# Kernel optimization log

Measured on AMD Instinct MI355X. Metric: run time of the kernel, lower is better.

The kernel has to match this reference:

```python
import jax, jax.numpy as jnp
import numpy as np

EPS = 1e-4      # geomloss: eps = blur**p = 0.01**2
N_ITERS = 20    # fixed Sinkhorn iterations
UNI_T = 2.0     # uniformity temperature (Wang & Isola)


def _sqdist(x, y):
    # [N,D],[M,D] -> [N,M] squared euclidean distances
    return jnp.sum((x[:, None, :] - y[None, :, :]) ** 2, axis=-1)


def _cost(x, y):
    # geomloss p=2 cost: ||x-y||^2 / 2
    return 0.5 * _sqdist(x, y)


def _softmin(C, h):
    # f_i = -eps * log( (1/M) * sum_j exp((h_j - C_ij)/eps) )
    M = C.shape[1]
    lse = jax.nn.logsumexp((h[None, :] - C) / EPS, axis=1)
    return -EPS * (lse - jnp.log(jnp.float32(M)))


def _sinkhorn_potentials(C):
    # alternating log-domain Sinkhorn updates, uniform weights
    def body(carry, _):
        f, g = carry
        f = _softmin(C, g)
        g = _softmin(C.T, f)
        return (f, g), None
    init = (jnp.zeros(C.shape[0], C.dtype), jnp.zeros(C.shape[1], C.dtype))
    (f, g), _ = jax.lax.scan(body, init, None, length=N_ITERS)
    return f, g


def _sym_potential(C):
    # symmetric fixed-point for the debiasing terms OT_eps(a,a)
    def body(p, _):
        return 0.5 * (p + _softmin(C, p)), None
    p, _ = jax.lax.scan(body, jnp.zeros(C.shape[0], C.dtype), None, length=N_ITERS)
    return p


def sinkhorn_divergence(x, y):
    # debiased: S = OT(x,y) - 0.5*OT(x,x) - 0.5*OT(y,y); envelope-theorem grads
    Cxy = _cost(x, y)
    f_d, g_d = _sinkhorn_potentials(jax.lax.stop_gradient(Cxy))
    f = _softmin(Cxy, jax.lax.stop_gradient(g_d))          # final differentiable step
    g = _softmin(Cxy.T, jax.lax.stop_gradient(f_d))

    Cxx = _cost(x, x)
    px = _sym_potential(jax.lax.stop_gradient(Cxx))
    fx = _softmin(Cxx, jax.lax.stop_gradient(px))          # 0.5*OT(x,x) = mean(fx)

    Cyy = _cost(y, y)
    py = _sym_potential(jax.lax.stop_gradient(Cyy))
    fy = _softmin(Cyy, jax.lax.stop_gradient(py))

    return jnp.mean(f) + jnp.mean(g) - jnp.mean(fx) - jnp.mean(fy)


def uniformity(x):
    # log E_{i != j} [ exp(-t * ||x_i - x_j||^2) ]
    N = x.shape[0]
    D = _sqdist(x, x)
    D = D + jnp.diag(jnp.full((N,), jnp.inf, dtype=x.dtype))  # mask self-pairs
    return jax.nn.logsumexp(-UNI_T * D) - jnp.log(jnp.float32(N * (N - 1)))


def setup_inputs() -> dict:
    key = jax.random.key(0)
    k1, k2 = jax.random.split(key)
    p_q = jax.random.normal(k1, (4096, 3), dtype=jnp.float32)
    p_gt = jax.random.normal(k2, (4096, 4), dtype=jnp.float32)
    return {"p_q": p_q, "p_gt": p_gt}


def reference(p_q, p_gt):
    L = sinkhorn_divergence(p_q, p_gt[:, :3])
    L = L + uniformity(p_q)
    return L
```

## Files before the change

### kernel.cpp

```cpp
#include <hip/hip_runtime.h>

#define NPT  4096
#define NBLK 256
#define NTHR 1024

constexpr float EPSV   = 1e-4f;
constexpr float LN2F   = 0.69314718055994531f;
constexpr float E2     = EPSV * LN2F;
constexpr float INV_E2 = 1.0f / E2;
constexpr float S_U    = 4.0f / LN2F;

#define SMEM_FLOATS 34816
#define SMEM_BYTES  (SMEM_FLOATS * 4)

#define WF     0
#define WG     4096
#define WPX0   8192
#define WPX1   12288
#define WPY0   16384
#define WPY1   20480
#define WFFIN  24576
#define WFXV   28672
#define WFYV   32768
#define WULS   36864
#define WCTR   40960
#define WREL   41472
#define WCNX   41984
#define WCNY   46080
#define WFG    50176
#define WGG    54272
#define WPXG0  58368
#define WPXG1  62464
#define WPYG0  66560
#define WPYG1  70656

typedef float v2f __attribute__((ext_vector_type(2)));

__device__ __forceinline__ float fexp2(float x) { return __builtin_amdgcn_exp2f(x); }
__device__ __forceinline__ float flog2(float x) { return __builtin_amdgcn_logf(x); }

__device__ __forceinline__ v2f pk_fma(v2f a, v2f b, v2f c) {
    v2f d;
    asm("v_pk_fma_f32 %0, %1, %2, %3" : "=v"(d) : "v"(a), "v"(b), "v"(c));
    return d;
}
__device__ __forceinline__ v2f pk_add(v2f a, v2f b) {
    v2f d;
    asm("v_pk_add_f32 %0, %1, %2" : "=v"(d) : "v"(a), "v"(b));
    return d;
}
__device__ __forceinline__ float max3f(float a, float b, float c) {
    float d;
    asm("v_max3_f32 %0, %1, %2, %3" : "=v"(d) : "v"(a), "v"(b), "v"(c));
    return d;
}

template<int CTRL>
__device__ __forceinline__ float dppf(float x) {
    return __int_as_float(__builtin_amdgcn_update_dpp(
        __float_as_int(x), __float_as_int(x), CTRL, 0xF, 0xF, false));
}

__device__ __forceinline__ float gload(const float* p) {
    return __hip_atomic_load(p, __ATOMIC_RELAXED, __HIP_MEMORY_SCOPE_SYSTEM);
}
__device__ __forceinline__ void gstore(float* p, float v) {
    __hip_atomic_store(p, v, __ATOMIC_RELAXED, __HIP_MEMORY_SCOPE_SYSTEM);
}
__device__ __forceinline__ float2 gload2(const float* p) {
    unsigned long long raw = __hip_atomic_load((const unsigned long long*)p,
                                               __ATOMIC_RELAXED, __HIP_MEMORY_SCOPE_SYSTEM);
    union { unsigned long long u; float2 f2; } cv; cv.u = raw;
    return cv.f2;
}

__device__ __forceinline__ void group_barrier(unsigned* ctr, unsigned* rel,
                                              unsigned tcnt, unsigned trel, int bb) {
    asm volatile("s_waitcnt vmcnt(0)" ::: "memory");
    __syncthreads();
    if (threadIdx.x == 0) {
        __hip_atomic_fetch_add(&ctr[(bb & 15) * 16], 1u,
                               __ATOMIC_RELAXED, __HIP_MEMORY_SCOPE_SYSTEM);
        if (bb == 0) {
            for (;;) {
                unsigned tot = 0;
#pragma unroll
                for (int i = 0; i < 16; ++i)
                    tot += __hip_atomic_load(&ctr[i * 16],
                                             __ATOMIC_RELAXED, __HIP_MEMORY_SCOPE_SYSTEM);
                if (tot >= tcnt) break;
                __builtin_amdgcn_s_sleep(1);
            }
            __hip_atomic_store(rel, trel, __ATOMIC_RELAXED, __HIP_MEMORY_SCOPE_SYSTEM);
        } else {
            while (__hip_atomic_load(rel, __ATOMIC_RELAXED, __HIP_MEMORY_SCOPE_SYSTEM) < trel)
                __builtin_amdgcn_s_sleep(1);
        }
    }
    __syncthreads();
}

template<bool ISU>
__device__ __forceinline__ void run_task(
    const float4* __restrict__ cpA, const float4* __restrict__ cpB,
    const float*  __restrict__ rAf, const float*  __restrict__ rBf,
    int r0g, int half, int lane, float scale, float2* part2, int lr0)
{
    v2f xs0[2], xs1[2], xs2[2];
#pragma unroll
    for (int r = 0; r < 2; ++r) {
        const int rr = r0g + r;
        const int pb4 = (rr >> 1) * 4, c0 = rr & 1;
        float xv = rAf[pb4 + c0] * scale;
        float yv = rAf[pb4 + 2 + c0] * scale;
        float zv = rBf[pb4 + c0] * scale;
        xs0[r] = (v2f){xv, xv};
        xs1[r] = (v2f){yv, yv};
        xs2[r] = (v2f){zv, zv};
    }
    float m[2], s[2];
    const int pbase = half * 1024 + lane;
    const float4* colA = cpA + pbase;
    const float4* colB = cpB + pbase;

#pragma unroll
    for (int chunk = 0; chunk < 4; ++chunk) {
        v2f av[2][4];
        float mc[2] = {-1e30f, -1e30f};
#pragma unroll
        for (int k = 0; k < 4; ++k) {
            const float4 a4 = colA[(chunk * 4 + k) * 64];
            const float4 b4 = colB[(chunk * 4 + k) * 64];
            const v2f xx = {a4.x, a4.y}, yy = {a4.z, a4.w};
            const v2f zz = {b4.x, b4.y}, gg = {b4.z, b4.w};
#pragma unroll
            for (int r = 0; r < 2; ++r) {
                v2f a01 = pk_fma(xs2[r], zz, gg);
                a01 = pk_fma(xs1[r], yy, a01);
                a01 = pk_fma(xs0[r], xx, a01);
                if (ISU) {
                    const int p = pbase + (chunk * 4 + k) * 64;
                    const int rr = r0g + r;
                    if (p == (rr >> 1)) {
                        if (rr & 1) a01.y = -1e30f; else a01.x = -1e30f;
                    }
                }
                av[r][k] = a01;
                mc[r] = max3f(mc[r], a01.x, a01.y);
            }
        }
#pragma unroll
        for (int r = 0; r < 2; ++r) {
            const float nm = -mc[r];
            v2f mcn = {nm, nm};
            float sA = 0.0f, sB = 0.0f;
#pragma unroll
            for (int k = 0; k < 4; ++k) {
                v2f d = pk_add(av[r][k], mcn);
                sA += fexp2(d.x);
                sB += fexp2(d.y);
            }
            const float sc_ = sA + sB;
            if (chunk == 0) { m[r] = mc[r]; s[r] = sc_; }
            else {
                float dd = m[r] - mc[r];
                float e = fexp2(-fabsf(dd));
                float bigs   = (dd >= 0.0f) ? s[r] : sc_;
                float smalls = (dd >= 0.0f) ? sc_  : s[r];
                s[r] = fmaf(smalls, e, bigs);
                m[r] = fmaxf(m[r], mc[r]);
            }
        }
    }
#pragma unroll
    for (int r = 0; r < 2; ++r) {
        const float ml = m[r];
        float mm = m[r];
        mm = fmaxf(mm, dppf<0xB1>(mm));
        mm = fmaxf(mm, dppf<0x4E>(mm));
        mm = fmaxf(mm, dppf<0x141>(mm));
        float ssv = s[r] * fexp2(ml - mm);
        ssv += dppf<0xB1>(ssv);
        ssv += dppf<0x4E>(ssv);
        ssv += dppf<0x141>(ssv);
        if ((lane & 7) == 0)
            part2[(lr0 + r) * 16 + half * 8 + (lane >> 3)] = make_float2(mm, ssv);
    }
}

__global__ void sink_init(const float* __restrict__ xin, const float* __restrict__ yin,
                          float* __restrict__ ws) {
    int t = blockIdx.x * blockDim.x + threadIdx.x;
    if (t < NPT) {
        gstore(ws + WF + t, 0.0f);
        gstore(ws + WG + t, 0.0f);
        gstore(ws + WPX0 + t, 0.0f);
        gstore(ws + WPY0 + t, 0.0f);
        float x0 = xin[3 * t], y0 = xin[3 * t + 1], z0 = xin[3 * t + 2];
        float cnx = 0.5f * (x0 * x0 + y0 * y0 + z0 * z0);
        float4 v = ((const float4*)yin)[t];
        float cny = 0.5f * (v.x * v.x + v.y * v.y + v.z * v.z);
        ws[WCNX + t] = cnx;
        ws[WCNY + t] = cny;
        gstore(ws + WGG   + t, -cny * INV_E2);
        gstore(ws + WPXG0 + t, -cnx * INV_E2);
        gstore(ws + WPYG0 + t, -cny * INV_E2);
    }
    if (t < 640) {
        __hip_atomic_store((unsigned*)(ws + WCTR) + t, 0u,
                           __ATOMIC_RELAXED, __HIP_MEMORY_SCOPE_SYSTEM);
    }
}

__global__ __launch_bounds__(NTHR)
__attribute__((amdgpu_waves_per_eu(4, 4)))
void sink_main(
    const float* __restrict__ xin, const float* __restrict__ yin,
    float* __restrict__ ws, float* __restrict__ out)
{
    extern __shared__ float smem[];
    float4* pAx = (float4*)smem;
    float4* pBx = (float4*)(smem + 8192);
    float4* pAy = (float4*)(smem + 16384);
    float4* pBy = (float4*)(smem + 24576);
    float2* part2 = (float2*)(smem + 32768);

    float* f    = ws + WF;
    float* g    = ws + WG;
    float* px0  = ws + WPX0;
    float* px1  = ws + WPX1;
    float* py0  = ws + WPY0;
    float* py1  = ws + WPY1;
    float* ffin = ws + WFFIN;
    float* fxv  = ws + WFXV;
    float* fyv  = ws + WFYV;
    float* uls  = ws + WULS;
    unsigned* ctrA = (unsigned*)(ws + WCTR);
    unsigned* ctrB = (unsigned*)(ws + WCTR) + 256;
    unsigned* relA = (unsigned*)(ws + WREL);
    unsigned* relB = (unsigned*)(ws + WREL) + 64;
    const float* cnx = ws + WCNX;
    const float* cny = ws + WCNY;
    float* fG   = ws + WFG;
    float* gG   = ws + WGG;
    float* pxG0 = ws + WPXG0;
    float* pxG1 = ws + WPXG1;
    float* pyG0 = ws + WPYG0;
    float* pyG1 = ws + WPYG1;

    const int tid  = threadIdx.x;
    const int b    = blockIdx.x;
    const int wave = tid >> 6;
    const int lane = tid & 63;
    const bool isA = b < 128;
    const int bb   = isA ? b : b - 128;
    unsigned* cctr = isA ? ctrA : ctrB;
    unsigned* crel = isA ? relA : relB;

    const float4* yin4 = (const float4*)yin;
    for (int i = tid; i < 2048; i += NTHR) {
        float x0 = xin[6 * i + 0], y0v = xin[6 * i + 1], z0 = xin[6 * i + 2];
        float x1 = xin[6 * i + 3], y1v = xin[6 * i + 4], z1 = xin[6 * i + 5];
        pAx[i] = make_float4(x0, x1, y0v, y1v);
        pBx[i] = make_float4(z0, z1, 0.0f, 0.0f);
        float4 v0 = yin4[2 * i], v1 = yin4[2 * i + 1];
        pAy[i] = make_float4(v0.x, v1.x, v0.y, v1.y);
        pBy[i] = make_float4(v0.z, v1.z, 0.0f, 0.0f);
    }
    __syncthreads();

    for (int h = 0; h <= 40; ++h) {
        bool rows_x, cols_x, isU = false, avg = false;
        const float* pot; const float* potG; float* outp; float* outpG;
        float scale = INV_E2;
        int row0g, rows_pb;
        if (h == 0) {
            if (b < 128)      { rows_x = true;  cols_x = false; pot = g;   potG = gG;   outp = f;   outpG = fG;   rows_pb = 32; row0g = b * 32; }
            else if (b < 192) { rows_x = true;  cols_x = true;  pot = px0; potG = pxG0; outp = px1; outpG = pxG1; avg = true; rows_pb = 64; row0g = (b - 128) * 64; }
            else              { rows_x = true;  cols_x = true;  pot = nullptr; potG = nullptr; outp = uls; outpG = nullptr; isU = true; scale = S_U; rows_pb = 64; row0g = (b - 192) * 64; }
        } else if (h == 40) {
            if (b < 128)      { rows_x = true;  cols_x = false; pot = g;   potG = gG;   outp = ffin; outpG = nullptr; rows_pb = 32; row0g = b * 32; }
            else if (b < 192) { rows_x = true;  cols_x = true;  pot = px0; potG = pxG0; outp = fxv;  outpG = nullptr; rows_pb = 64; row0g = (b - 128) * 64; }
            else              { rows_x = false; cols_x = false; pot = py0; potG = pyG0; outp = fyv;  outpG = nullptr; rows_pb = 64; row0g = (b - 192) * 64; }
        } else if (h & 1) {
            int k = (h - 1) >> 1;
            if (b < 128) { rows_x = false; cols_x = true;  pot = f; potG = fG; outp = g; outpG = gG; rows_pb = 32; row0g = b * 32; }
            else         { rows_x = false; cols_x = false;
                           pot  = (k & 1) ? py1  : py0;  potG  = (k & 1) ? pyG1 : pyG0;
                           outp = (k & 1) ? py0  : py1;  outpG = (k & 1) ? pyG0 : pyG1;
                           avg = true; rows_pb = 32; row0g = (b - 128) * 32; }
        } else {
            int k = h >> 1;
            if (b < 128) { rows_x = true; cols_x = false; pot = g; potG = gG; outp = f; outpG = fG; rows_pb = 32; row0g = b * 32; }
            else         { rows_x = true; cols_x = true;
                           pot  = (k & 1) ? px1  : px0;  potG  = (k & 1) ? pxG1 : pxG0;
                           outp = (k & 1) ? px0  : px1;  outpG = (k & 1) ? pxG0 : pxG1;
                           avg = true; rows_pb = 32; row0g = (b - 128) * 32; }
        }

        float4* cpA = cols_x ? pAx : pAy;
        float4* cpB = cols_x ? pBx : pBy;
        const float* ccn = cols_x ? cnx : cny;
        for (int p = tid; p < 2048; p += NTHR) {
            float2 g2;
            if (isU) {
                float2 cn2 = ((const float2*)ccn)[p];
                g2 = make_float2(-cn2.x * S_U, -cn2.y * S_U);
            } else {
                g2 = gload2(potG + 2 * p);
            }
            ((float2*)&cpB[p])[1] = g2;
        }
        __syncthreads();

        const float* rAf = (const float*)(rows_x ? pAx : pAy);
        const float* rBf = (const float*)(rows_x ? pBx : pBy);
        const int ntask = rows_pb;
        for (int t = wave; t < ntask; t += 16) {
            int grp = t >> 1, half = t & 1;
            int lr0 = grp << 1;
            int r0g = row0g + lr0;
            if (isU) run_task<true >(cpA, cpB, rAf, rBf, r0g, half, lane, scale, part2, lr0);
            else     run_task<false>(cpA, cpB, rAf, rBf, r0g, half, lane, scale, part2, lr0);
        }
        __syncthreads();

        const float* rcn = rows_x ? cnx : cny;
        if (tid < rows_pb) {
            float2 pv2[16];
#pragma unroll
            for (int q = 0; q < 16; ++q) pv2[q] = part2[tid * 16 + q];
            float mm = pv2[0].x;
#pragma unroll
            for (int q = 1; q < 15; q += 2) mm = max3f(mm, pv2[q].x, pv2[q + 1].x);
            mm = fmaxf(mm, pv2[15].x);
            float ss = 0.0f;
#pragma unroll
            for (int q = 0; q < 16; ++q) ss += pv2[q].y * fexp2(pv2[q].x - mm);
            int rg = row0g + tid;
            float rn = rcn[rg];
            float lse2 = mm + flog2(ss) - rn * scale;
            float val;
            if (isU) {
                val = lse2;
            } else {
                val = -E2 * (lse2 - 12.0f);
                if (avg) val = 0.5f * (gload(pot + rg) + val);
            }
            gstore(outp + rg, val);
            if (outpG) gstore(outpG + rg, (val - rn) * INV_E2);
        }

        group_barrier(cctr, crel, 128u * (unsigned)(h + 1), (unsigned)(h + 1), bb);
    }

    if (b == 0) {
        if (tid == 0) {
            while (__hip_atomic_load(relB, __ATOMIC_RELAXED, __HIP_MEMORY_SCOPE_SYSTEM) < 41u)
                __builtin_amdgcn_s_sleep(1);
        }
        __syncthreads();

        float sf = 0.f, sg = 0.f, sx = 0.f, sy = 0.f, um = -1e30f, us = 0.f;
        for (int i = tid; i < NPT; i += NTHR) {
            sf += gload(ffin + i); sg += gload(g + i);
            sx += gload(fxv + i);  sy += gload(fyv + i);
            float v = gload(uls + i);
            float mn = fmaxf(um, v);
            us = us * fexp2(um - mn) + fexp2(v - mn);
            um = mn;
        }
#pragma unroll
        for (int off = 1; off < 64; off <<= 1) {
            sf += __shfl_xor(sf, off, 64);
            sg += __shfl_xor(sg, off, 64);
            sx += __shfl_xor(sx, off, 64);
            sy += __shfl_xor(sy, off, 64);
            float mo = __shfl_xor(um, off, 64);
            float so = __shfl_xor(us, off, 64);
            float mn = fmaxf(um, mo);
            us = us * fexp2(um - mn) + so * fexp2(mo - mn);
            um = mn;
        }
        __syncthreads();
        if (lane == 0) {
            float* red = smem;
            red[wave * 6 + 0] = sf; red[wave * 6 + 1] = sg; red[wave * 6 + 2] = sx;
            red[wave * 6 + 3] = sy; red[wave * 6 + 4] = um; red[wave * 6 + 5] = us;
        }
        __syncthreads();
        if (tid == 0) {
            float* red = smem;
            float Sf = 0, Sg = 0, Sx = 0, Sy = 0, Um = -1e30f, Us = 0;
            for (int w = 0; w < 16; ++w) {
                Sf += red[w * 6 + 0]; Sg += red[w * 6 + 1];
                Sx += red[w * 6 + 2]; Sy += red[w * 6 + 3];
                float mo = red[w * 6 + 4], so = red[w * 6 + 5];
                float mn = fmaxf(Um, mo);
                Us = Us * fexp2(Um - mn) + so * fexp2(mo - mn);
                Um = mn;
            }
            float mean = (Sf + Sg - Sx - Sy) * (1.0f / 4096.0f);
            float U = LN2F * (Um + flog2(Us)) - logf(4096.0f * 4095.0f);
            out[0] = mean + U;
        }
    }
}

extern "C" void kernel_launch(void* const* d_in, const int* in_sizes, int n_in,
                              void* d_out, int out_size, void* d_ws, size_t ws_size,
                              hipStream_t stream) {
    const float* x = (const float*)d_in[0];
    const float* y = (const float*)d_in[1];
    float* ws  = (float*)d_ws;
    float* out = (float*)d_out;

    (void)hipFuncSetAttribute((const void*)sink_main,
                              hipFuncAttributeMaxDynamicSharedMemorySize, SMEM_BYTES);

    sink_init<<<4, 1024, 0, stream>>>(x, y, ws);
    sink_main<<<NBLK, NTHR, SMEM_BYTES, stream>>>(x, y, ws, out);
}
```

Before: 482.6 us.

## Process four rows per wave task with op_sel packed FMAs and online softmax

Each wave task now covers four rows instead of two, so every column float4 loaded from LDS is reused across twice as many rows. Row coordinates are packed in pairs and broadcast through op_sel/op_sel_hi on v_pk_fma_f32, which removes the duplicated splat registers. The chunked max/sum merge becomes a per-chunk online logsumexp over smaller chunks in a non-unrolled loop. This trades lower LDS traffic and less task overhead for higher register pressure and an extra exp per chunk, and it halves the number of tasks available for the 16 waves.

```diff
diff --git a/kernel.cpp b/kernel.cpp
--- a/kernel.cpp
+++ b/kernel.cpp
@@ -39,9 +39,16 @@
 __device__ __forceinline__ float fexp2(float x) { return __builtin_amdgcn_exp2f(x); }
 __device__ __forceinline__ float flog2(float x) { return __builtin_amdgcn_logf(x); }
 
-__device__ __forceinline__ v2f pk_fma(v2f a, v2f b, v2f c) {
+__device__ __forceinline__ v2f pk_fma_lo(v2f a, v2f b, v2f c) {
     v2f d;
-    asm("v_pk_fma_f32 %0, %1, %2, %3" : "=v"(d) : "v"(a), "v"(b), "v"(c));
+    asm("v_pk_fma_f32 %0, %1, %2, %3 op_sel:[0,0,0] op_sel_hi:[0,1,1]"
+        : "=v"(d) : "v"(a), "v"(b), "v"(c));
+    return d;
+}
+__device__ __forceinline__ v2f pk_fma_hi(v2f a, v2f b, v2f c) {
+    v2f d;
+    asm("v_pk_fma_f32 %0, %1, %2, %3 op_sel:[1,0,0] op_sel_hi:[1,1,1]"
+        : "=v"(d) : "v"(a), "v"(b), "v"(c));
     return d;
 }
 __device__ __forceinline__ v2f pk_add(v2f a, v2f b) {
@@ -106,74 +113,70 @@
     const float*  __restrict__ rAf, const float*  __restrict__ rBf,
     int r0g, int half, int lane, float scale, float2* part2, int lr0)
 {
-    v2f xs0[2], xs1[2], xs2[2];
-#pragma unroll
-    for (int r = 0; r < 2; ++r) {
-        const int rr = r0g + r;
-        const int pb4 = (rr >> 1) * 4, c0 = rr & 1;
-        float xv = rAf[pb4 + c0] * scale;
-        float yv = rAf[pb4 + 2 + c0] * scale;
-        float zv = rBf[pb4 + c0] * scale;
-        xs0[r] = (v2f){xv, xv};
-        xs1[r] = (v2f){yv, yv};
-        xs2[r] = (v2f){zv, zv};
-    }
-    float m[2], s[2];
+    const int q4 = (r0g >> 1) * 4;
+    v2f xsA0 = {rAf[q4 + 0] * scale, rAf[q4 + 1] * scale};
+    v2f xsA1 = {rAf[q4 + 2] * scale, rAf[q4 + 3] * scale};
+    v2f xsA2 = {rBf[q4 + 0] * scale, rBf[q4 + 1] * scale};
+    v2f xsB0 = {rAf[q4 + 4] * scale, rAf[q4 + 5] * scale};
+    v2f xsB1 = {rAf[q4 + 6] * scale, rAf[q4 + 7] * scale};
+    v2f xsB2 = {rBf[q4 + 4] * scale, rBf[q4 + 5] * scale};
+
+    float m[4] = {-1e30f, -1e30f, -1e30f, -1e30f};
+    float s[4] = {0.0f, 0.0f, 0.0f, 0.0f};
     const int pbase = half * 1024 + lane;
     const float4* colA = cpA + pbase;
     const float4* colB = cpB + pbase;
 
-#pragma unroll
-    for (int chunk = 0; chunk < 4; ++chunk) {
-        v2f av[2][4];
-        float mc[2] = {-1e30f, -1e30f};
-#pragma unroll
-        for (int k = 0; k < 4; ++k) {
-            const float4 a4 = colA[(chunk * 4 + k) * 64];
-            const float4 b4 = colB[(chunk * 4 + k) * 64];
+#pragma unroll 1
+    for (int c = 0; c < 8; ++c) {
+        v2f av[4][2];
+#pragma unroll
+        for (int k = 0; k < 2; ++k) {
+            const float4 a4 = colA[(c * 2 + k) * 64];
+            const float4 b4 = colB[(c * 2 + k) * 64];
             const v2f xx = {a4.x, a4.y}, yy = {a4.z, a4.w};
             const v2f zz = {b4.x, b4.y}, gg = {b4.z, b4.w};
-#pragma unroll
-            for (int r = 0; r < 2; ++r) {
-                v2f a01 = pk_fma(xs2[r], zz, gg);
-                a01 = pk_fma(xs1[r], yy, a01);
-                a01 = pk_fma(xs0[r], xx, a01);
-                if (ISU) {
-                    const int p = pbase + (chunk * 4 + k) * 64;
+            v2f t0 = pk_fma_lo(xsA2, zz, gg);
+            t0 = pk_fma_lo(xsA1, yy, t0);
+            t0 = pk_fma_lo(xsA0, xx, t0);
+            v2f t1 = pk_fma_hi(xsA2, zz, gg);
+            t1 = pk_fma_hi(xsA1, yy, t1);
+            t1 = pk_fma_hi(xsA0, xx, t1);
+            v2f t2 = pk_fma_lo(xsB2, zz, gg);
+            t2 = pk_fma_lo(xsB1, yy, t2);
+            t2 = pk_fma_lo(xsB0, xx, t2);
+            v2f t3 = pk_fma_hi(xsB2, zz, gg);
+            t3 = pk_fma_hi(xsB1, yy, t3);
+            t3 = pk_fma_hi(xsB0, xx, t3);
+            if (ISU) {
+                const int p = pbase + (c * 2 + k) * 64;
+#pragma unroll
+                for (int r = 0; r < 4; ++r) {
                     const int rr = r0g + r;
                     if (p == (rr >> 1)) {
-                        if (rr & 1) a01.y = -1e30f; else a01.x = -1e30f;
+                        v2f* tv = (r == 0) ? &t0 : (r == 1) ? &t1 : (r == 2) ? &t2 : &t3;
+                        if (rr & 1) tv->y = -1e30f; else tv->x = -1e30f;
                     }
                 }
-                av[r][k] = a01;
-                mc[r] = max3f(mc[r], a01.x, a01.y);
             }
-        }
-#pragma unroll
-        for (int r = 0; r < 2; ++r) {
-            const float nm = -mc[r];
-            v2f mcn = {nm, nm};
-            float sA = 0.0f, sB = 0.0f;
-#pragma unroll
-            for (int k = 0; k < 4; ++k) {
-                v2f d = pk_add(av[r][k], mcn);
-                sA += fexp2(d.x);
-                sB += fexp2(d.y);
-            }
-            const float sc_ = sA + sB;
-            if (chunk == 0) { m[r] = mc[r]; s[r] = sc_; }
-            else {
-                float dd = m[r] - mc[r];
-                float e = fexp2(-fabsf(dd));
-                float bigs   = (dd >= 0.0f) ? s[r] : sc_;
-                float smalls = (dd >= 0.0f) ? sc_  : s[r];
-                s[r] = fmaf(smalls, e, bigs);
-                m[r] = fmaxf(m[r], mc[r]);
-            }
-        }
-    }
-#pragma unroll
-    for (int r = 0; r < 2; ++r) {
+            av[0][k] = t0; av[1][k] = t1; av[2][k] = t2; av[3][k] = t3;
+        }
+#pragma unroll
+        for (int r = 0; r < 4; ++r) {
+            float mc = max3f(av[r][0].x, av[r][0].y, av[r][1].x);
+            mc = fmaxf(mc, av[r][1].y);
+            const float mn = fmaxf(m[r], mc);
+            const float e = fexp2(m[r] - mn);
+            v2f nm2 = {-mn, -mn};
+            v2f d0 = pk_add(av[r][0], nm2);
+            v2f d1 = pk_add(av[r][1], nm2);
+            float sc_ = fexp2(d0.x) + fexp2(d0.y) + fexp2(d1.x) + fexp2(d1.y);
+            s[r] = fmaf(s[r], e, sc_);
+            m[r] = mn;
+        }
+    }
+#pragma unroll
+    for (int r = 0; r < 4; ++r) {
         const float ml = m[r];
         float mm = m[r];
         mm = fmaxf(mm, dppf<0xB1>(mm));
@@ -315,10 +318,10 @@
 
         const float* rAf = (const float*)(rows_x ? pAx : pAy);
         const float* rBf = (const float*)(rows_x ? pBx : pBy);
-        const int ntask = rows_pb;
+        const int ntask = rows_pb >> 1;
         for (int t = wave; t < ntask; t += 16) {
             int grp = t >> 1, half = t & 1;
-            int lr0 = grp << 1;
+            int lr0 = grp << 2;
             int r0g = row0g + lr0;
             if (isU) run_task<true >(cpA, cpB, rAf, rBf, r0g, half, lane, scale, part2, lr0);
             else     run_task<false>(cpA, cpB, rAf, rBf, r0g, half, lane, scale, part2, lr0);
```

After: 463.9 us. -3.9%, faster.
